# Kernel optimization log

Measured on AMD Instinct MI355X. Metric: run time of the kernel, lower is better.

The kernel has to match this reference:

```python
import jax, jax.numpy as jnp
import numpy as np

COMMITMENT_COST = 0.25


def setup_inputs() -> dict:
    key = jax.random.key(0)
    k1, k2 = jax.random.split(key)
    N, K, D = 131072, 1024, 64
    inputs = jax.random.normal(k1, (N, D), dtype=jnp.float32)
    # torch init: uniform(-1/K, 1/K); use randn scaled similarly-small for a generic table
    embedding = jax.random.uniform(k2, (K, D), dtype=jnp.float32,
                                   minval=-1.0 / K, maxval=1.0 / K)
    return {"inputs": inputs, "embedding": embedding}


def reference(inputs, embedding):
    distances = (jnp.sum(inputs ** 2, axis=1, keepdims=True)
                 + jnp.sum(embedding ** 2, axis=1)
                 - 2.0 * inputs @ embedding.T)
    encoding_indices = jnp.argmin(distances, axis=1)            # [N]
    # direct gather (same math as one-hot @ embedding)
    quantized = embedding[encoding_indices]                     # [N, D]

    diff2 = jnp.mean((quantized - inputs) ** 2)
    # e_latent_loss == q_latent_loss numerically in fwd
    loss = diff2 + COMMITMENT_COST * diff2

    # straight-through output (forward value == quantized)
    quantized_st = inputs + jax.lax.stop_gradient(quantized - inputs)

    # avg_probs via histogram instead of materializing [N, K] one-hot
    N, K = inputs.shape[0], embedding.shape[0]
    counts = jnp.zeros((K,), dtype=jnp.float32).at[encoding_indices].add(1.0)
    avg_probs = counts / N
    perplexity = jnp.exp(-jnp.sum(avg_probs * jnp.log(avg_probs + 1e-10)))

    return quantized_st, loss, encoding_indices.reshape(N, 1), perplexity
```

## Files before the change

kernel.cpp:

```cpp
#include <hip/hip_runtime.h>
#include <hip/hip_bf16.h>

#define D 64
#define MARGIN 4e-5f
#define KS 2

typedef __attribute__((ext_vector_type(8))) short bf16x8;
typedef __attribute__((ext_vector_type(4))) float f32x4;
typedef __attribute__((ext_vector_type(4))) unsigned uint4v;


__device__ __forceinline__ float np_pairwise_sumsq64(const float* a) {
    float r[8];
#pragma unroll
    for (int j = 0; j < 8; ++j) r[j] = __fmul_rn(a[j], a[j]);
#pragma unroll
    for (int i = 8; i < 64; i += 8)
#pragma unroll
        for (int j = 0; j < 8; ++j)
            r[j] = __fadd_rn(r[j], __fmul_rn(a[i + j], a[i + j]));
    return __fadd_rn(
        __fadd_rn(__fadd_rn(r[0], r[1]), __fadd_rn(r[2], r[3])),
        __fadd_rn(__fadd_rn(r[4], r[5]), __fadd_rn(r[6], r[7])));
}

#define CVT8(F0, F1, H, L)                                                    \
    do {                                                                      \
        float _f[8] = {F0.x, F0.y, F0.z, F0.w, F1.x, F1.y, F1.z, F1.w};       \
        _Pragma("unroll") for (int _i = 0; _i < 8; ++_i) {                    \
            unsigned _u = __float_as_uint(_f[_i]);                            \
            unsigned _hb = (_u + 0x7fffu + ((_u >> 16) & 1u)) >> 16;          \
            float _hf = __uint_as_float(_hb << 16);                           \
            float _r = _f[_i] - _hf;                                          \
            unsigned _u2 = __float_as_uint(_r);                               \
            unsigned _lb = (_u2 + 0x7fffu + ((_u2 >> 16) & 1u)) >> 16;        \
            H[_i] = (short)_hb;                                               \
            L[_i] = (short)_lb;                                               \
        }                                                                     \
    } while (0)

__global__ __launch_bounds__(256) void vq_prep_all(
    const float* __restrict__ emb, int K,
    float* __restrict__ eenp, float* __restrict__ neh,
    unsigned short* __restrict__ ehs, float* __restrict__ eT) {
    int b = blockIdx.x;
    if (b < 64) {
        int t = b * 256 + threadIdx.x;
        int tile = t >> 8, r = t & 255, s = r >> 6, l = r & 63;
        int sub = l & 15, grp = l >> 4;
        int k = tile * 16 + sub;
        int d0 = ((s & 1) << 5) + (grp << 3);
        const float* e = emb + (size_t)k * D + d0;
        float4 f0 = *(const float4*)e;
        float4 f1 = *(const float4*)(e + 4);
        bf16x8 h, lo;
        CVT8(f0, f1, h, lo);
        *(bf16x8*)(ehs + (size_t)t * 8) = (s >> 1) ? lo : h;
    } else if (b < 68) {
        int k = (b - 64) * 256 + threadIdx.x;
        float s = np_pairwise_sumsq64(emb + (size_t)k * D);
        eenp[k] = s;
        neh[k] = -0.5f * s;
    } else {
        int t = (b - 68) * 256 + threadIdx.x;
        int d = t / K, k = t - d * K;
        eT[t] = emb[(size_t)k * D + d];
    }
}

__global__ __launch_bounds__(256) void vq_screen(
    const float* __restrict__ x, const unsigned short* __restrict__ ehs,
    const float* __restrict__ neh, int N, int K,
    float* __restrict__ m1p, float* __restrict__ m2p, int* __restrict__ bip,
    float* __restrict__ xxp) {
    const int tid = threadIdx.x;
    const int lane = tid & 63;
    const int wid = tid >> 6;
    const int kslice = blockIdx.x & (KS - 1);
    const int rowblk = blockIdx.x >> 1;
    const int row0 = rowblk * 256 + wid * 64;
    const int sub = lane & 15, grp = lane >> 4;
    const int g4 = grp << 2;
    const int k0 = kslice * (K / KS);
    const int NT = (K / KS) >> 4;
    const int t0 = k0 >> 4;

    __shared__ __align__(16) unsigned short lds[2][2048];

    bf16x8 xh[4][2], xl[4][2];
    float xq[4];
#pragma unroll
    for (int rt = 0; rt < 4; ++rt) {
        xq[rt] = 0.f;
        const float* xrow = x + (((size_t)(row0 + (rt << 4) + sub)) << 6) + (grp << 3);
#pragma unroll
        for (int s = 0; s < 2; ++s) {
            float4 f0 = *(const float4*)(xrow + (s << 5));
            float4 f1 = *(const float4*)(xrow + (s << 5) + 4);
            xq[rt] = fmaf(f0.x, f0.x, xq[rt]); xq[rt] = fmaf(f0.y, f0.y, xq[rt]);
            xq[rt] = fmaf(f0.z, f0.z, xq[rt]); xq[rt] = fmaf(f0.w, f0.w, xq[rt]);
            xq[rt] = fmaf(f1.x, f1.x, xq[rt]); xq[rt] = fmaf(f1.y, f1.y, xq[rt]);
            xq[rt] = fmaf(f1.z, f1.z, xq[rt]); xq[rt] = fmaf(f1.w, f1.w, xq[rt]);
            CVT8(f0, f1, xh[rt][s], xl[rt][s]);
        }
    }
#pragma unroll
    for (int rt = 0; rt < 4; ++rt) {
        xq[rt] += __shfl_xor(xq[rt], 16);
        xq[rt] += __shfl_xor(xq[rt], 32);
    }

    float m1[4], m2[4];
    int bi[4];
#pragma unroll
    for (int rt = 0; rt < 4; ++rt) { m1[rt] = -3e38f; m2[rt] = -3e38f; bi[rt] = 0; }

    const unsigned short* sbase = ehs + ((size_t)t0 << 11);
    const int slot = (wid << 9) + (lane << 3);

    uint4v tmp = *(const uint4v*)(sbase + slot);
    *(uint4v*)&lds[0][slot] = tmp;
    __syncthreads();

    for (int t = 0; t < NT; ++t) {
        const int cur = t & 1;
        if (t + 1 < NT)
            tmp = *(const uint4v*)(sbase + ((size_t)(t + 1) << 11) + slot);

        f32x4 cb = *(const f32x4*)(neh + k0 + (t << 4) + g4);
        const bf16x8* L = (const bf16x8*)&lds[cur][0];
        bf16x8 a0 = L[lane];
        bf16x8 a1 = L[64 + lane];
        bf16x8 a2 = L[128 + lane];
        bf16x8 a3 = L[192 + lane];

        f32x4 acc[4];
#pragma unroll
        for (int rt = 0; rt < 4; ++rt)
            acc[rt] = __builtin_amdgcn_mfma_f32_16x16x32_bf16(a0, xh[rt][0], cb, 0, 0, 0);
#pragma unroll
        for (int rt = 0; rt < 4; ++rt)
            acc[rt] = __builtin_amdgcn_mfma_f32_16x16x32_bf16(a2, xh[rt][0], acc[rt], 0, 0, 0);
#pragma unroll
        for (int rt = 0; rt < 4; ++rt)
            acc[rt] = __builtin_amdgcn_mfma_f32_16x16x32_bf16(a0, xl[rt][0], acc[rt], 0, 0, 0);
#pragma unroll
        for (int rt = 0; rt < 4; ++rt)
            acc[rt] = __builtin_amdgcn_mfma_f32_16x16x32_bf16(a1, xh[rt][1], acc[rt], 0, 0, 0);
#pragma unroll
        for (int rt = 0; rt < 4; ++rt)
            acc[rt] = __builtin_amdgcn_mfma_f32_16x16x32_bf16(a3, xh[rt][1], acc[rt], 0, 0, 0);
#pragma unroll
        for (int rt = 0; rt < 4; ++rt)
            acc[rt] = __builtin_amdgcn_mfma_f32_16x16x32_bf16(a1, xl[rt][1], acc[rt], 0, 0, 0);

        int cbase = k0 + (t << 4) + g4;
#pragma unroll
        for (int rt = 0; rt < 4; ++rt) {
#pragma unroll
            for (int j = 0; j < 4; ++j) {
                float v = acc[rt][j];
                int c = cbase + j;
                bool tk = v > m1[rt];
                m2[rt] = fminf(fmaxf(v, m2[rt]), m1[rt]);
                m1[rt] = tk ? v : m1[rt];
                bi[rt] = tk ? c : bi[rt];
            }
        }

        if (t + 1 < NT)
            *(uint4v*)&lds[cur ^ 1][slot] = tmp;
        __syncthreads();
    }

#pragma unroll
    for (int rt = 0; rt < 4; ++rt) {
#pragma unroll
        for (int off = 16; off <= 32; off <<= 1) {
            float om1 = __shfl_xor(m1[rt], off);
            float om2 = __shfl_xor(m2[rt], off);
            int obi = __shfl_xor(bi[rt], off);
            bool take = (om1 > m1[rt]) || (om1 == m1[rt] && obi < bi[rt]);
            m2[rt] = fmaxf(fminf(om1, m1[rt]), fmaxf(om2, m2[rt]));
            m1[rt] = take ? om1 : m1[rt];
            bi[rt] = take ? obi : bi[rt];
        }
    }

    if (lane < 16) {
#pragma unroll
        for (int rt = 0; rt < 4; ++rt) {
            size_t idx = (size_t)kslice * N + row0 + (rt << 4) + lane;
            m1p[idx] = m1[rt];
            m2p[idx] = m2[rt];
            bip[idx] = bi[rt];
            if (kslice == 0) xxp[row0 + (rt << 4) + lane] = xq[rt];
        }
    }
}

__global__ __launch_bounds__(256) void vq_epilogue(
    const float* __restrict__ x, const float* __restrict__ emb,
    const float* __restrict__ eT, const float* __restrict__ eenp,
    const float* __restrict__ m1p, const float* __restrict__ m2p,
    const int* __restrict__ bip, const float* __restrict__ xxp, int N, int K,
    float* __restrict__ outq, float* __restrict__ outidx,
    double* __restrict__ lossA) {
    const int tid = threadIdx.x;
    const int rows0 = blockIdx.x * 64;
    __shared__ int sdec[64];
    __shared__ int samb[64];
    __shared__ int snamb;
    __shared__ float sxrow[64];
    __shared__ float swm[4];
    __shared__ int swi[4];

    double lacc = 0.0;

    if (tid < 64) {
        int r = rows0 + tid;
        float gm1 = m1p[r], gm2 = m2p[r];
        int gbi = bip[r];
        {
            size_t idx = (size_t)N + r;
            float m1b = m1p[idx], m2b = m2p[idx];
            int bb = bip[idx];
            bool take = m1b > gm1;
            gm2 = fmaxf(fminf(gm1, m1b), fmaxf(gm2, m2b));
            gm1 = take ? m1b : gm1;
            gbi = take ? bb : gbi;
        }
        bool amb = 2.0f * (gm1 - gm2) < MARGIN;
        unsigned long long mask = __ballot(amb);
        int dec = gbi;
        double lpart = 0.0;
        if (amb) {
            int rank = __popcll(mask & ((1ull << tid) - 1ull));
            samb[rank] = tid;
            dec = -1;
        } else {
            outidx[r] = (float)dec;
            lpart = (double)(xxp[r] - 2.0f * gm1);
        }
        sdec[tid] = dec;
        if (tid == 0) snamb = __popcll(mask);
#pragma unroll
        for (int off = 32; off; off >>= 1) lpart += __shfl_down(lpart, off);
        if (tid == 0) lacc = lpart;
    }
    __syncthreads();

    const int namb = snamb;
    const int w = tid >> 6, l = tid & 63;
    const f32x4* eT4 = (const f32x4*)eT;
    for (int j = 0; j < namb; ++j) {
        int lr = samb[j];
        int row = rows0 + lr;
        if (tid < 64) sxrow[tid] = x[(size_t)row * D + tid];
        __syncthreads();
        float xx = np_pairwise_sumsq64(sxrow);
        f32x4 dt = (f32x4){0.f, 0.f, 0.f, 0.f};
#pragma unroll 8
        for (int d = 0; d < D; ++d) {
            f32x4 ev = eT4[(size_t)d * 256 + tid];
            float xv = sxrow[d];
            dt[0] = __fmaf_rn(xv, ev[0], dt[0]);
            dt[1] = __fmaf_rn(xv, ev[1], dt[1]);
            dt[2] = __fmaf_rn(xv, ev[2], dt[2]);
            dt[3] = __fmaf_rn(xv, ev[3], dt[3]);
        }
        float bm = 1e30f;
        int bi = 0;
#pragma unroll
        for (int jj = 0; jj < 4; ++jj) {
            int k = (tid << 2) + jj;
            float dist = __fsub_rn(__fadd_rn(xx, eenp[k]),
                                   __fmul_rn(2.0f, dt[jj]));
            if (dist < bm) { bm = dist; bi = k; }
        }
#pragma unroll
        for (int off = 1; off < 64; off <<= 1) {
            float ov = __shfl_xor(bm, off);
            int oi = __shfl_xor(bi, off);
            if (ov < bm || (ov == bm && oi < bi)) { bm = ov; bi = oi; }
        }
        if (l == 0) { swm[w] = bm; swi[w] = bi; }
        __syncthreads();
        if (tid == 0) {
            float fm = swm[0];
            int fi = swi[0];
#pragma unroll
            for (int ww = 1; ww < 4; ++ww) {
                float ov = swm[ww];
                int oi = swi[ww];
                if (ov < fm || (ov == fm && oi < fi)) { fm = ov; fi = oi; }
            }
            sdec[lr] = fi;
            outidx[row] = (float)fi;
            lacc += (double)fm;
        }
        __syncthreads();
    }
    if (tid == 0) lossA[blockIdx.x] = lacc;

    const int chunk = tid & 15, rl = tid >> 4;
#pragma unroll
    for (int p = 0; p < 4; ++p) {
        int lr = p * 16 + rl;
        int dp = sdec[lr];
        if (dp >= 0) {
            float4 ev = *(const float4*)(emb + (size_t)dp * D + chunk * 4);
            *(float4*)(outq + (size_t)(rows0 + lr) * D + chunk * 4) = ev;
        }
    }
}

__global__ __launch_bounds__(256) void vq_histperp(
    const float* __restrict__ outidx, int N, int K,
    unsigned* __restrict__ counts, unsigned* __restrict__ done,
    const double* __restrict__ lossA, int nA,
    float* __restrict__ out_loss, float* __restrict__ out_perp) {
    __shared__ unsigned h[1024];
    __shared__ unsigned rank_s;
#pragma unroll
    for (int i = 0; i < 4; ++i) h[threadIdx.x + 256 * i] = 0;
    __syncthreads();
    int per = N / gridDim.x;
    int base = blockIdx.x * per;
    for (int i = threadIdx.x; i < per; i += 256) {
        int k = (int)outidx[base + i];
        atomicAdd(&h[k], 1u);
    }
    __syncthreads();
#pragma unroll
    for (int i = 0; i < 4; ++i) {
        int b = threadIdx.x + 256 * i;
        unsigned v = h[b];
        if (b < K && v) atomicAdd(counts + b, v);
    }
    __threadfence();
    if (threadIdx.x == 0) rank_s = atomicAdd(done, 1u);
    __syncthreads();
    if (rank_s == gridDim.x - 1) {
        double part = 0.0;
        for (int k = threadIdx.x; k < K; k += 256) {
            unsigned c = atomicAdd(counts + k, 0u);
            double p = (double)c / (double)N;
            part += p * log(p + 1e-10);
        }
        double lsum = 0.0;
        for (int i = threadIdx.x; i < nA; i += 256) lsum += lossA[i];
#pragma unroll
        for (int off = 32; off; off >>= 1) {
            part += __shfl_down(part, off);
            lsum += __shfl_down(lsum, off);
        }
        __shared__ double ls[4], ls2[4];
        if ((threadIdx.x & 63) == 0) {
            ls[threadIdx.x >> 6] = part;
            ls2[threadIdx.x >> 6] = lsum;
        }
        __syncthreads();
        if (threadIdx.x == 0) {
            double s = ls[0] + ls[1] + ls[2] + ls[3];
            double L = ls2[0] + ls2[1] + ls2[2] + ls2[3];
            *out_perp = (float)exp(-s);
            *out_loss = (float)(1.25 * (L / ((double)N * (double)D)));
        }
    }
}

extern "C" void kernel_launch(void* const* d_in, const int* in_sizes, int n_in,
                              void* d_out, int out_size, void* d_ws, size_t ws_size,
                              hipStream_t stream) {
    const float* x = (const float*)d_in[0];
    const float* emb = (const float*)d_in[1];
    int N = in_sizes[0] / D;
    int K = in_sizes[1] / D;

    float* outq = (float*)d_out;
    float* out_loss = outq + (size_t)N * D;
    float* outidx = out_loss + 1;
    float* out_perp = outidx + N;

    char* ws = (char*)d_ws;
    unsigned* counts = (unsigned*)ws;
    unsigned* done = (unsigned*)(ws + (size_t)K * 4);
    size_t off = (size_t)K * 4 + 16;
    float* neh = (float*)(ws + off);            off += (size_t)K * 4;
    float* eenp = (float*)(ws + off);           off += (size_t)K * 4;
    unsigned short* ehs = (unsigned short*)(ws + off);  off += (size_t)K * 256;
    float* eT = (float*)(ws + off);              off += (size_t)K * D * 4;
    float* m1p = (float*)(ws + off);             off += (size_t)KS * N * 4;
    float* m2p = (float*)(ws + off);             off += (size_t)KS * N * 4;
    int* bip = (int*)(ws + off);                 off += (size_t)KS * N * 4;
    float* xxp = (float*)(ws + off);             off += (size_t)N * 4;
    int nA = N / 64;
    double* lossA = (double*)(ws + off);         off += (size_t)nA * 8;

    hipMemsetAsync(d_ws, 0, (size_t)K * 4 + 16, stream);

    vq_prep_all<<<64 + 4 + (K * D + 255) / 256, 256, 0, stream>>>(
        emb, K, eenp, neh, ehs, eT);
    vq_screen<<<(N / 256) * KS, 256, 0, stream>>>(x, ehs, neh, N, K,
                                                  m1p, m2p, bip, xxp);
    vq_epilogue<<<N / 64, 256, 0, stream>>>(x, emb, eT, eenp, m1p, m2p, bip,
                                            xxp, N, K, outq, outidx, lossA);
    vq_histperp<<<16, 256, 0, stream>>>(outidx, N, K, counts, done,
                                        lossA, nA, out_loss, out_perp);
}
```

Measured before the change: 164.4 us.

## Fuse histogram and perplexity into epilogue, zero workspace in prep kernel

Removes the separate histogram/perplexity kernel and the memset by zeroing counters in an extra prep block. The epilogue now does global atomic count increments per row and a fixed-point atomic loss sum, and the last block to finish computes the perplexity and loss. This saves two launches and a reread of the indices, at the cost of many global atomics on 1024 counters and fixed-point loss rounding. The prep grid size is hardcoded to 325, which assumes K=1024.

```diff
diff --git a/kernel.cpp b/kernel.cpp
--- a/kernel.cpp
+++ b/kernel.cpp
@@ -4,6 +4,7 @@
 #define D 64
 #define MARGIN 4e-5f
 #define KS 2
+#define LSCALE 274877906944.0
 
 typedef __attribute__((ext_vector_type(8))) short bf16x8;
 typedef __attribute__((ext_vector_type(4))) float f32x4;
@@ -42,7 +43,9 @@
 __global__ __launch_bounds__(256) void vq_prep_all(
     const float* __restrict__ emb, int K,
     float* __restrict__ eenp, float* __restrict__ neh,
-    unsigned short* __restrict__ ehs, float* __restrict__ eT) {
+    unsigned short* __restrict__ ehs, float* __restrict__ eT,
+    unsigned* __restrict__ counts, unsigned* __restrict__ done,
+    unsigned long long* __restrict__ lossU) {
     int b = blockIdx.x;
     if (b < 64) {
         int t = b * 256 + threadIdx.x;
@@ -61,10 +64,17 @@
         float s = np_pairwise_sumsq64(emb + (size_t)k * D);
         eenp[k] = s;
         neh[k] = -0.5f * s;
-    } else {
+    } else if (b < 324) {
         int t = (b - 68) * 256 + threadIdx.x;
         int d = t / K, k = t - d * K;
         eT[t] = emb[(size_t)k * D + d];
+    } else {
+#pragma unroll
+        for (int i = 0; i < 4; ++i) {
+            int c = threadIdx.x + 256 * i;
+            if (c < K) counts[c] = 0u;
+        }
+        if (threadIdx.x == 0) { *done = 0u; *lossU = 0ull; }
     }
 }
 
@@ -205,7 +215,9 @@
     const float* __restrict__ m1p, const float* __restrict__ m2p,
     const int* __restrict__ bip, const float* __restrict__ xxp, int N, int K,
     float* __restrict__ outq, float* __restrict__ outidx,
-    double* __restrict__ lossA) {
+    unsigned* __restrict__ counts, unsigned* __restrict__ done,
+    unsigned long long* __restrict__ lossU,
+    float* __restrict__ out_loss, float* __restrict__ out_perp) {
     const int tid = threadIdx.x;
     const int rows0 = blockIdx.x * 64;
     __shared__ int sdec[64];
@@ -214,6 +226,7 @@
     __shared__ float sxrow[64];
     __shared__ float swm[4];
     __shared__ int swi[4];
+    __shared__ unsigned rank_s;
 
     double lacc = 0.0;
 
@@ -301,69 +314,38 @@
         }
         __syncthreads();
     }
-    if (tid == 0) lossA[blockIdx.x] = lacc;
+
+    if (tid < 64) atomicAdd(counts + sdec[tid], 1u);
+    if (tid == 0)
+        atomicAdd(lossU, (unsigned long long)(lacc * LSCALE + 0.5));
 
     const int chunk = tid & 15, rl = tid >> 4;
 #pragma unroll
     for (int p = 0; p < 4; ++p) {
         int lr = p * 16 + rl;
         int dp = sdec[lr];
-        if (dp >= 0) {
-            float4 ev = *(const float4*)(emb + (size_t)dp * D + chunk * 4);
-            *(float4*)(outq + (size_t)(rows0 + lr) * D + chunk * 4) = ev;
-        }
-    }
-}
-
-__global__ __launch_bounds__(256) void vq_histperp(
-    const float* __restrict__ outidx, int N, int K,
-    unsigned* __restrict__ counts, unsigned* __restrict__ done,
-    const double* __restrict__ lossA, int nA,
-    float* __restrict__ out_loss, float* __restrict__ out_perp) {
-    __shared__ unsigned h[1024];
-    __shared__ unsigned rank_s;
-#pragma unroll
-    for (int i = 0; i < 4; ++i) h[threadIdx.x + 256 * i] = 0;
-    __syncthreads();
-    int per = N / gridDim.x;
-    int base = blockIdx.x * per;
-    for (int i = threadIdx.x; i < per; i += 256) {
-        int k = (int)outidx[base + i];
-        atomicAdd(&h[k], 1u);
-    }
-    __syncthreads();
-#pragma unroll
-    for (int i = 0; i < 4; ++i) {
-        int b = threadIdx.x + 256 * i;
-        unsigned v = h[b];
-        if (b < K && v) atomicAdd(counts + b, v);
-    }
+        float4 ev = *(const float4*)(emb + (size_t)dp * D + chunk * 4);
+        *(float4*)(outq + (size_t)(rows0 + lr) * D + chunk * 4) = ev;
+    }
+
     __threadfence();
-    if (threadIdx.x == 0) rank_s = atomicAdd(done, 1u);
+    if (tid == 0) rank_s = atomicAdd(done, 1u);
     __syncthreads();
     if (rank_s == gridDim.x - 1) {
         double part = 0.0;
-        for (int k = threadIdx.x; k < K; k += 256) {
+        for (int k = tid; k < K; k += 256) {
             unsigned c = atomicAdd(counts + k, 0u);
             double p = (double)c / (double)N;
             part += p * log(p + 1e-10);
         }
-        double lsum = 0.0;
-        for (int i = threadIdx.x; i < nA; i += 256) lsum += lossA[i];
-#pragma unroll
-        for (int off = 32; off; off >>= 1) {
-            part += __shfl_down(part, off);
-            lsum += __shfl_down(lsum, off);
-        }
-        __shared__ double ls[4], ls2[4];
-        if ((threadIdx.x & 63) == 0) {
-            ls[threadIdx.x >> 6] = part;
-            ls2[threadIdx.x >> 6] = lsum;
-        }
-        __syncthreads();
-        if (threadIdx.x == 0) {
+#pragma unroll
+        for (int off = 32; off; off >>= 1) part += __shfl_down(part, off);
+        __shared__ double ls[4];
+        if ((tid & 63) == 0) ls[tid >> 6] = part;
+        __syncthreads();
+        if (tid == 0) {
             double s = ls[0] + ls[1] + ls[2] + ls[3];
-            double L = ls2[0] + ls2[1] + ls2[2] + ls2[3];
+            double L = (double)atomicAdd(lossU, 0ull) / LSCALE;
             *out_perp = (float)exp(-s);
             *out_loss = (float)(1.25 * (L / ((double)N * (double)D)));
         }
@@ -386,6 +368,8 @@
     char* ws = (char*)d_ws;
     unsigned* counts = (unsigned*)ws;
     unsigned* done = (unsigned*)(ws + (size_t)K * 4);
+    unsigned long long* lossU =
+        (unsigned long long*)(ws + (size_t)K * 4 + 8);
     size_t off = (size_t)K * 4 + 16;
     float* neh = (float*)(ws + off);            off += (size_t)K * 4;
     float* eenp = (float*)(ws + off);           off += (size_t)K * 4;
@@ -395,17 +379,13 @@
     float* m2p = (float*)(ws + off);             off += (size_t)KS * N * 4;
     int* bip = (int*)(ws + off);                 off += (size_t)KS * N * 4;
     float* xxp = (float*)(ws + off);             off += (size_t)N * 4;
-    int nA = N / 64;
-    double* lossA = (double*)(ws + off);         off += (size_t)nA * 8;
-
-    hipMemsetAsync(d_ws, 0, (size_t)K * 4 + 16, stream);
-
-    vq_prep_all<<<64 + 4 + (K * D + 255) / 256, 256, 0, stream>>>(
-        emb, K, eenp, neh, ehs, eT);
+
+    vq_prep_all<<<325, 256, 0, stream>>>(emb, K, eenp, neh, ehs, eT,
+                                         counts, done, lossU);
     vq_screen<<<(N / 256) * KS, 256, 0, stream>>>(x, ehs, neh, N, K,
                                                   m1p, m2p, bip, xxp);
     vq_epilogue<<<N / 64, 256, 0, stream>>>(x, emb, eT, eenp, m1p, m2p, bip,
-                                            xxp, N, K, outq, outidx, lossA);
-    vq_histperp<<<16, 256, 0, stream>>>(outidx, N, K, counts, done,
-                                        lossA, nA, out_loss, out_perp);
-}
+                                            xxp, N, K, outq, outidx,
+                                            counts, done, lossU,
+                                            out_loss, out_perp);
+}
```

After: 346.7 us. +110.9%, slower.
